# Performance work log

Measured on AMD Instinct MI355X. Metric: run time of the kernel, lower is better.

## Reference

```python
import jax, jax.numpy as jnp
import numpy as np

XBOUND = (-51.2, 51.2, 0.8)
YBOUND = (-51.2, 51.2, 0.8)
ZBOUND = (-10.0, 10.0, 20.0)
DBOUND = (1.0, 60.0, 1.0)
IMG_H, IMG_W = 256, 704
DOWNSAMPLE = 16
CAM_C = 64
OUT_C = 64
D = int((DBOUND[1] - DBOUND[0]) / DBOUND[2])      # 59
NX = int((XBOUND[1] - XBOUND[0]) / XBOUND[2])     # 128
NY = int((YBOUND[1] - YBOUND[0]) / YBOUND[2])     # 128
NZ = int((ZBOUND[1] - ZBOUND[0]) / ZBOUND[2])     # 1
FH, FW = IMG_H // DOWNSAMPLE, IMG_W // DOWNSAMPLE # 16, 44
DX = jnp.array([XBOUND[2], YBOUND[2], ZBOUND[2]], dtype=jnp.float32)
BX = jnp.array([XBOUND[0] + XBOUND[2] / 2.0, YBOUND[0] + YBOUND[2] / 2.0, ZBOUND[0] + ZBOUND[2] / 2.0], dtype=jnp.float32)


def make_frustum():
    ds = jnp.arange(DBOUND[0], DBOUND[1], DBOUND[2], dtype=jnp.float32)   # [D]
    xs = jnp.linspace(0.0, IMG_W - 1.0, FW, dtype=jnp.float32)            # [FW]
    ys = jnp.linspace(0.0, IMG_H - 1.0, FH, dtype=jnp.float32)            # [FH]
    d = jnp.broadcast_to(ds[:, None, None], (D, FH, FW))
    x = jnp.broadcast_to(xs[None, None, :], (D, FH, FW))
    y = jnp.broadcast_to(ys[None, :, None], (D, FH, FW))
    return jnp.stack([x, y, d], axis=-1)                                  # [D,FH,FW,3]


def get_geometry(rots, trans, intrins, post_rots, post_trans):
    # rots/intrins/post_rots: [B,N,3,3]; trans/post_trans: [B,N,3]
    frustum = make_frustum()                                              # [D,FH,FW,3]
    pts = frustum[None, None] - post_trans[:, :, None, None, None]        # [B,N,D,FH,FW,3]
    pts = jnp.einsum('bnij,bndhwj->bndhwi', jnp.linalg.inv(post_rots), pts)
    pts = jnp.concatenate([pts[..., :2] * pts[..., 2:3], pts[..., 2:3]], axis=-1)
    comb = jnp.matmul(rots, jnp.linalg.inv(intrins))
    pts = jnp.einsum('bnij,bndhwj->bndhwi', comb, pts)
    return pts + trans[:, :, None, None, None]


def forward(x, rots, trans, intrins, post_rots, post_trans, w_depth, b_depth):
    B, N, C_in, H, W = x.shape
    # 1x1 conv == channel matmul
    y = jnp.einsum('bnchw,oc->bnohw', x, w_depth) + b_depth[None, None, :, None, None]
    depth = jax.nn.softmax(y[:, :, :D], axis=2)              # [B,N,D,H,W]
    context = y[:, :, D:]                                    # [B,N,OUT_C,H,W]
    outer = depth[:, :, :, None] * context[:, :, None, :]    # [B,N,D,OUT_C,H,W]
    outer = jnp.transpose(outer, (0, 1, 2, 4, 5, 3))         # [B,N,D,H,W,OUT_C]

    geom = jax.lax.stop_gradient(get_geometry(rots, trans, intrins, post_rots, post_trans))
    # torch .long() truncates toward zero -> jnp.trunc
    g = jnp.trunc((geom.reshape(-1, 3) - (BX - DX / 2.0)) / DX).astype(jnp.int32)  # [P,3]
    kept = ((g[:, 0] >= 0) & (g[:, 0] < NX) &
            (g[:, 1] >= 0) & (g[:, 1] < NY) &
            (g[:, 2] >= 0) & (g[:, 2] < NZ))
    batch_ix = jnp.repeat(jnp.arange(B, dtype=jnp.int32), N * D * H * W)
    ranks = batch_ix * (NX * NY * NZ) + g[:, 0] + g[:, 1] * NX + g[:, 2] * NX * NY
    # segment-sum over voxel ranks == sort+cumsum trick + scatter in the original
    feats = jnp.where(kept[:, None], outer.reshape(-1, OUT_C), 0.0)
    ranks = jnp.where(kept, ranks, 0)
    bev = jax.ops.segment_sum(feats, ranks, num_segments=B * NZ * NY * NX)
    bev = bev.reshape(B, NZ, NY, NX, OUT_C).transpose(0, 4, 1, 2, 3).sum(axis=2)
    return bev  # [B, OUT_C, NY, NX]


def setup_inputs() -> dict:
    key = jax.random.key(0)
    B, N = 4, 6
    ks = jax.random.split(key, 8)
    cam2ego = jnp.array([[0.0, 0.0, 1.0], [-1.0, 0.0, 0.0], [0.0, -1.0, 0.0]], dtype=jnp.float32)
    rots = jnp.broadcast_to(cam2ego, (B, N, 3, 3)) + 0.02 * jax.random.normal(ks[0], (B, N, 3, 3), dtype=jnp.float32)
    trans = 1.0 * jax.random.normal(ks[1], (B, N, 3), dtype=jnp.float32)
    K = jnp.array([[700.0, 0.0, IMG_W / 2.0], [0.0, 700.0, IMG_H / 2.0], [0.0, 0.0, 1.0]], dtype=jnp.float32)
    intrins = jnp.broadcast_to(K, (B, N, 3, 3)) + 0.1 * jax.random.normal(ks[2], (B, N, 3, 3), dtype=jnp.float32)
    post_rots = jnp.broadcast_to(jnp.eye(3, dtype=jnp.float32), (B, N, 3, 3)) + 0.01 * jax.random.normal(ks[3], (B, N, 3, 3), dtype=jnp.float32)
    post_trans = 0.1 * jax.random.normal(ks[4], (B, N, 3), dtype=jnp.float32)
    x = jax.random.normal(ks[5], (B, N, CAM_C, FH, FW), dtype=jnp.float32)
    w_depth = 0.05 * jax.random.normal(ks[6], (D + OUT_C, CAM_C), dtype=jnp.float32)
    b_depth = jnp.zeros((D + OUT_C,), dtype=jnp.float32)
    return {"x": x, "rots": rots, "trans": trans, "intrins": intrins,
            "post_rots": post_rots, "post_trans": post_trans,
            "w_depth": w_depth, "b_depth": b_depth}


def reference(x, rots, trans, intrins, post_rots, post_trans, w_depth, b_depth):
    return forward(x, rots, trans, intrins, post_rots, post_trans, w_depth, b_depth)
```

## Files before the change

kernel.cpp:

```cpp
#include <hip/hip_runtime.h>
#include <math.h>

#define Bc 4
#define Nc 6
#define Dc 59
#define FHc 16
#define FWc 44
#define Cc 64
#define OCc 123
#define NXc 128
#define NYc 128
#define NVOX (Bc*NXc*NYc)
#define NBLK (Bc*Nc*FWc)

#define WS_ACC 0
#define WS_CAM ((size_t)16777216)
#define WS_WDT ((size_t)16781312)

template<bool FMA>
__device__ __forceinline__ float mulsub(float a, float b, float c) {
    if (FMA) return __fmaf_rn(-a, b, c);
    return __fadd_rn(c, __fmul_rn(-a, b));
}

template<bool FMA>
__device__ __forceinline__ void lu_inv3x3T(const float* __restrict__ m, float* __restrict__ o) {
    float A[3][3] = {{m[0],m[3],m[6]},{m[1],m[4],m[7]},{m[2],m[5],m[8]}};
    int piv0, piv1;
    {
        float a0=fabsf(A[0][0]), a1=fabsf(A[1][0]), a2=fabsf(A[2][0]);
        int p = 0; float mx = a0;
        if (a1 > mx) { mx = a1; p = 1; }
        if (a2 > mx) { mx = a2; p = 2; }
        piv0 = p;
        if (p != 0) { for (int k=0;k<3;++k){ float t=A[0][k]; A[0][k]=A[p][k]; A[p][k]=t; } }
        const float d = __fdiv_rn(1.0f, A[0][0]);
        A[1][0] = __fmul_rn(A[1][0], d);
        A[2][0] = __fmul_rn(A[2][0], d);
        #pragma unroll
        for (int i=1;i<3;++i)
            #pragma unroll
            for (int j=1;j<3;++j)
                A[i][j] = mulsub<FMA>(A[i][0], A[0][j], A[i][j]);
    }
    {
        float a1=fabsf(A[1][1]), a2=fabsf(A[2][1]);
        int p = (a2 > a1) ? 2 : 1;
        piv1 = p;
        if (p != 1) { for (int k=0;k<3;++k){ float t=A[1][k]; A[1][k]=A[p][k]; A[p][k]=t; } }
        const float d = __fdiv_rn(1.0f, A[1][1]);
        A[2][1] = __fmul_rn(A[2][1], d);
        A[2][2] = mulsub<FMA>(A[2][1], A[1][2], A[2][2]);
    }
    float B[3][3] = {{1.f,0.f,0.f},{0.f,1.f,0.f},{0.f,0.f,1.f}};
    if (piv0 != 0) { for (int k=0;k<3;++k){ float t=B[0][k]; B[0][k]=B[piv0][k]; B[piv0][k]=t; } }
    if (piv1 != 1) { for (int k=0;k<3;++k){ float t=B[1][k]; B[1][k]=B[piv1][k]; B[piv1][k]=t; } }
    #pragma unroll
    for (int j=0;j<3;++j) {
        B[1][j] = mulsub<FMA>(A[1][0], B[0][j], B[1][j]);
        B[2][j] = mulsub<FMA>(A[2][0], B[0][j], B[2][j]);
        B[2][j] = mulsub<FMA>(A[2][1], B[1][j], B[2][j]);
        B[2][j] = __fdiv_rn(B[2][j], A[2][2]);
        B[0][j] = mulsub<FMA>(A[0][2], B[2][j], B[0][j]);
        B[1][j] = mulsub<FMA>(A[1][2], B[2][j], B[1][j]);
        B[1][j] = __fdiv_rn(B[1][j], A[1][1]);
        B[0][j] = mulsub<FMA>(A[0][1], B[1][j], B[0][j]);
        B[0][j] = __fdiv_rn(B[0][j], A[0][0]);
    }
    o[0]=B[0][0]; o[1]=B[1][0]; o[2]=B[2][0];
    o[3]=B[0][1]; o[4]=B[1][1]; o[5]=B[2][1];
    o[6]=B[0][2]; o[7]=B[1][2]; o[8]=B[2][2];
}

template<bool FMA>
__device__ __forceinline__ float dot3(float a0,float a1,float a2,float b0,float b1,float b2){
    if (FMA) return __fmaf_rn(a2,b2, __fmaf_rn(a1,b1, __fmul_rn(a0,b0)));
    return __fadd_rn(__fadd_rn(__fmul_rn(a0,b0), __fmul_rn(a1,b1)), __fmul_rn(a2,b2));
}

__global__ __launch_bounds__(256) void prep(
    const float* __restrict__ wd, const float* __restrict__ rots,
    const float* __restrict__ intrins, const float* __restrict__ post_rots,
    float* __restrict__ wdT2, float* __restrict__ camMat)
{
    const int idx = blockIdx.x*256 + threadIdx.x;
    if (idx < OCc*Cc) {
        const int o = idx >> 6, c = idx & 63;
        const int slot = (o < 64) ? (o << 1) : (((o - 64) << 1) | 1);
        wdT2[(c << 7) + slot] = wd[idx];
    }
    if (idx >= OCc*Cc && idx < OCc*Cc + 320) {
        const int k = idx - OCc*Cc;
        const int c = k / 5, o = 59 + (k % 5);
        wdT2[(c << 7) + (o << 1) + 1] = 0.0f;
    }
    if (blockIdx.x == 0 && threadIdx.x < 48) {
        const int cam = threadIdx.x >> 1;
        const int var = threadIdx.x & 1;
        const float* pr = post_rots + cam*9;
        const float* ro = rots      + cam*9;
        const float* it = intrins   + cam*9;
        float PRi[9], INi[9], CM[9];
        if (var == 0) { lu_inv3x3T<true >(pr, PRi); lu_inv3x3T<true >(it, INi); }
        else          { lu_inv3x3T<false>(pr, PRi); lu_inv3x3T<false>(it, INi); }
        #pragma unroll
        for (int r2 = 0; r2 < 3; ++r2)
            #pragma unroll
            for (int c2 = 0; c2 < 3; ++c2)
                CM[r2*3+c2] = dot3<true>(ro[r2*3+0], ro[r2*3+1], ro[r2*3+2],
                                         INi[0*3+c2], INi[1*3+c2], INi[2*3+c2]);
        float* dst = camMat + (size_t)(cam*2 + var)*18;
        #pragma unroll
        for (int k = 0; k < 9; ++k) { dst[k] = PRi[k]; dst[9+k] = CM[k]; }
    }
}

template<bool FMA>
__device__ __forceinline__ int geom_light(
    const float* __restrict__ PRi, const float* __restrict__ CM,
    float pt0, float pt1, float pt2, float tr0, float tr1, float tr2,
    float u, float v, float dval, int b)
{
    const float p0 = __fsub_rn(u,    pt0);
    const float p1 = __fsub_rn(v,    pt1);
    const float p2 = __fsub_rn(dval, pt2);
    const float q0 = dot3<FMA>(PRi[0],PRi[1],PRi[2], p0,p1,p2);
    const float q1 = dot3<FMA>(PRi[3],PRi[4],PRi[5], p0,p1,p2);
    const float q2 = dot3<FMA>(PRi[6],PRi[7],PRi[8], p0,p1,p2);
    const float r0 = __fmul_rn(q0, q2);
    const float r1 = __fmul_rn(q1, q2);
    const float s0 = __fadd_rn(dot3<FMA>(CM[0],CM[1],CM[2], r0,r1,q2), tr0);
    const float s1 = __fadd_rn(dot3<FMA>(CM[3],CM[4],CM[5], r0,r1,q2), tr1);
    const float s2 = __fadd_rn(dot3<FMA>(CM[6],CM[7],CM[8], r0,r1,q2), tr2);
    const float CX  = -51.200000762939453f;
    const float DXf =  0.80000001192092896f;
    const float gx = __fdiv_rn(__fsub_rn(s0, CX), DXf);
    const float gy = __fdiv_rn(__fsub_rn(s1, CX), DXf);
    const float gz = __fdiv_rn(__fsub_rn(s2, -10.0f), 20.0f);
    const bool kept = (gx > -1.0f) && (gx < 128.0f) &&
                      (gy > -1.0f) && (gy < 128.0f) &&
                      (gz > -1.0f) && (gz < 1.0f);
    return kept ? (b*(NXc*NYc) + ((int)gy)*NXc + (int)gx) : -1;
}

__global__ __launch_bounds__(256, 4) void lss_main(
    const float* __restrict__ x, const float* __restrict__ trans,
    const float* __restrict__ post_trans, const float* __restrict__ bd,
    const float* __restrict__ wdT2, const float* __restrict__ camMat,
    float* __restrict__ acc)
{
    const int blk = blockIdx.x;
    const int wi  = blk % FWc;
    const int cam = blk / FWc;
    const int b   = cam / Nc;
    const int t = threadIdx.x;
    const int wave = t >> 6, lane = t & 63;

    __shared__ float  xsT[64][16];
    __shared__ float  yv[16][60];
    __shared__ float  ctxT[64][18];
    __shared__ float4 geo[Dc][16];

    {
        const float* xb = x + (size_t)cam*64*(FHc*FWc) + wi;
        for (int idx = t; idx < 1024; idx += 256) {
            const int c = idx >> 4, hi = idx & 15;
            xsT[c][hi] = xb[(size_t)c*(FHc*FWc) + hi*FWc];
        }
    }
    __syncthreads();

    {
        const int hi0 = wave << 2;
        float a0[4] = {0.f,0.f,0.f,0.f}, a1[4] = {0.f,0.f,0.f,0.f};
        const float2* wrow = (const float2*)wdT2 + lane;
        #pragma unroll 8
        for (int c = 0; c < 64; ++c) {
            const float2 wv = wrow[c << 6];
            const float4 xv = *(const float4*)&xsT[c][hi0];
            a0[0] = __fmaf_rn(wv.x, xv.x, a0[0]); a1[0] = __fmaf_rn(wv.y, xv.x, a1[0]);
            a0[1] = __fmaf_rn(wv.x, xv.y, a0[1]); a1[1] = __fmaf_rn(wv.y, xv.y, a1[1]);
            a0[2] = __fmaf_rn(wv.x, xv.z, a0[2]); a1[2] = __fmaf_rn(wv.y, xv.z, a1[2]);
            a0[3] = __fmaf_rn(wv.x, xv.w, a0[3]); a1[3] = __fmaf_rn(wv.y, xv.w, a1[3]);
        }
        const float b0 = bd[lane];
        const float b1 = (lane < 59) ? bd[64 + lane] : 0.0f;
        #pragma unroll
        for (int k = 0; k < 4; ++k) {
            const int hi = hi0 + k;
            const float y0 = __fadd_rn(a0[k], b0);
            if (lane < 59) {
                yv[hi][lane] = y0;
                ctxT[lane + 5][hi] = __fadd_rn(a1[k], b1);
            } else {
                ctxT[lane - 59][hi] = y0;
            }
        }
    }
    for (int k = 0; k < 4; ++k) {
        const int hi = (wave << 2) | k;
        float v = (lane < Dc) ? yv[hi][lane] : -INFINITY;
        float m = v;
        #pragma unroll
        for (int off = 32; off; off >>= 1) m = fmaxf(m, __shfl_xor(m, off));
        float e = (lane < Dc) ? expf(__fsub_rn(v, m)) : 0.0f;
        float s = e;
        #pragma unroll
        for (int off = 32; off; off >>= 1) s = __fadd_rn(s, __shfl_xor(s, off));
        if (lane < Dc) yv[hi][lane] = __fdiv_rn(e, s);
    }
    __syncthreads();

    {
        const float pt0 = post_trans[cam*3+0], pt1 = post_trans[cam*3+1], pt2 = post_trans[cam*3+2];
        const float tr0 = trans[cam*3+0],      tr1 = trans[cam*3+1],      tr2 = trans[cam*3+2];
        const float* M0 = camMat + (size_t)(cam*2 + 0)*18;
        const float* M1 = camMat + (size_t)(cam*2 + 1)*18;
        const float u = (float)(wi * (703.0 / 43.0));
        for (int idx = t; idx < 16*Dc; idx += 256) {
            const int d = idx >> 4, hi = idx & 15;
            const float v    = (float)(hi * 17.0);
            const float dval = (float)(1 + d);
            const int vA = geom_light<true >(M0, M0+9, pt0,pt1,pt2, tr0,tr1,tr2, u, v, dval, b);
            const int vB = geom_light<false>(M1, M1+9, pt0,pt1,pt2, tr0,tr1,tr2, u, v, dval, b);
            geo[d][hi] = make_float4(yv[hi][d], __int_as_float(vA), __int_as_float(vB), 0.0f);
        }
    }
    __syncthreads();

    {
        float cx[16];
        #pragma unroll
        for (int h = 0; h < 16; h += 2) {
            const float2 c2 = *(const float2*)&ctxT[lane][h];
            cx[h] = c2.x; cx[h+1] = c2.y;
        }
        for (int d = wave; d < Dc; d += 4) {
            int runVox = -1;
            float accv = 0.0f;
            #pragma unroll
            for (int hi = 0; hi < 16; ++hi) {
                const float4 g = geo[d][hi];
                const float dw = g.x;
                const int vA = __float_as_int(g.y);
                const int vB = __float_as_int(g.z);
                const float cxv = cx[hi];
                if (vA == vB) {
                    if (vA >= 0) {
                        if (vA != runVox) {
                            if (runVox >= 0) atomicAdd(&acc[((size_t)runVox << 6) + lane], accv);
                            runVox = vA; accv = 0.0f;
                        }
                        accv = __fadd_rn(accv, __fmul_rn(dw, cxv));
                    }
                } else {
                    const float hw = __fmul_rn(dw, 0.5f);
                    if (vA >= 0) {
                        if (vA != runVox) {
                            if (runVox >= 0) atomicAdd(&acc[((size_t)runVox << 6) + lane], accv);
                            runVox = vA; accv = 0.0f;
                        }
                        accv = __fadd_rn(accv, __fmul_rn(hw, cxv));
                    }
                    if (vB >= 0) atomicAdd(&acc[((size_t)vB << 6) + lane], __fmul_rn(hw, cxv));
                }
            }
            if (runVox >= 0) atomicAdd(&acc[((size_t)runVox << 6) + lane], accv);
        }
    }
}

__global__ __launch_bounds__(256) void lss_transpose(
    const float* __restrict__ acc, float* __restrict__ out)
{
    __shared__ float tile[64][65];
    const int blk = blockIdx.x;
    const int b = blk >> 8;
    const int pixbase = (blk & 255) * 64;
    const float* src = acc + ((size_t)b*16384 + pixbase)*64;
    const int t = threadIdx.x;
    #pragma unroll
    for (int i = 0; i < 16; ++i) {
        const int e = i*256 + t;
        tile[e & 63][e >> 6] = src[e];
    }
    __syncthreads();
    float* dst = out + (size_t)b*64*16384 + pixbase;
    #pragma unroll
    for (int i = 0; i < 16; ++i) {
        const int e = i*256 + t;
        const int c = e >> 6, p = e & 63;
        dst[(size_t)c*16384 + p] = tile[c][p];
    }
}

extern "C" void kernel_launch(void* const* d_in, const int* in_sizes, int n_in,
                              void* d_out, int out_size, void* d_ws, size_t ws_size,
                              hipStream_t stream) {
    const float* x          = (const float*)d_in[0];
    const float* rots       = (const float*)d_in[1];
    const float* trans      = (const float*)d_in[2];
    const float* intrins    = (const float*)d_in[3];
    const float* post_rots  = (const float*)d_in[4];
    const float* post_trans = (const float*)d_in[5];
    const float* wd         = (const float*)d_in[6];
    const float* bd         = (const float*)d_in[7];
    float* out = (float*)d_out;
    char* ws = (char*)d_ws;

    float* acc    = (float*)(ws + WS_ACC);
    float* camMat = (float*)(ws + WS_CAM);
    float* wdT2   = (float*)(ws + WS_WDT);

    hipMemsetAsync(acc, 0, (size_t)NVOX*64*sizeof(float), stream);
    prep<<<dim3(32), dim3(256), 0, stream>>>(wd, rots, intrins, post_rots, wdT2, camMat);
    lss_main<<<dim3(NBLK), dim3(256), 0, stream>>>(
        x, trans, post_trans, bd, wdT2, camMat, acc);
    lss_transpose<<<dim3(Bc*256), dim3(256), 0, stream>>>(acc, out);
}
```

Baseline: 203.6 us.

## Fuse memset, prep, scatter and transpose into one kernel with grid barriers

Replaces the memset, prep kernel, main scatter kernel and transpose kernel with a single persistent kernel. Phases are separated by software grid barriers on atomic counters that use a poison-value convention for first-arrival initialisation. It also zeroes the accumulator in-kernel with float4 stores and vectorises the transpose loads and stores. The aim is to remove launch and inter-kernel gaps, but correctness relies on all 1056 blocks being co-resident and on the counter workspace being re-poisoned before every call.

```diff
diff --git a/kernel.cpp b/kernel.cpp
--- a/kernel.cpp
+++ b/kernel.cpp
@@ -16,6 +16,8 @@
 #define WS_ACC 0
 #define WS_CAM ((size_t)16777216)
 #define WS_WDT ((size_t)16781312)
+#define WS_CNT ((size_t)16814080)
+#define POISON 0xAAAAAAAAu
 
 template<bool FMA>
 __device__ __forceinline__ float mulsub(float a, float b, float c) {
@@ -76,43 +78,6 @@
 __device__ __forceinline__ float dot3(float a0,float a1,float a2,float b0,float b1,float b2){
     if (FMA) return __fmaf_rn(a2,b2, __fmaf_rn(a1,b1, __fmul_rn(a0,b0)));
     return __fadd_rn(__fadd_rn(__fmul_rn(a0,b0), __fmul_rn(a1,b1)), __fmul_rn(a2,b2));
-}
-
-__global__ __launch_bounds__(256) void prep(
-    const float* __restrict__ wd, const float* __restrict__ rots,
-    const float* __restrict__ intrins, const float* __restrict__ post_rots,
-    float* __restrict__ wdT2, float* __restrict__ camMat)
-{
-    const int idx = blockIdx.x*256 + threadIdx.x;
-    if (idx < OCc*Cc) {
-        const int o = idx >> 6, c = idx & 63;
-        const int slot = (o < 64) ? (o << 1) : (((o - 64) << 1) | 1);
-        wdT2[(c << 7) + slot] = wd[idx];
-    }
-    if (idx >= OCc*Cc && idx < OCc*Cc + 320) {
-        const int k = idx - OCc*Cc;
-        const int c = k / 5, o = 59 + (k % 5);
-        wdT2[(c << 7) + (o << 1) + 1] = 0.0f;
-    }
-    if (blockIdx.x == 0 && threadIdx.x < 48) {
-        const int cam = threadIdx.x >> 1;
-        const int var = threadIdx.x & 1;
-        const float* pr = post_rots + cam*9;
-        const float* ro = rots      + cam*9;
-        const float* it = intrins   + cam*9;
-        float PRi[9], INi[9], CM[9];
-        if (var == 0) { lu_inv3x3T<true >(pr, PRi); lu_inv3x3T<true >(it, INi); }
-        else          { lu_inv3x3T<false>(pr, PRi); lu_inv3x3T<false>(it, INi); }
-        #pragma unroll
-        for (int r2 = 0; r2 < 3; ++r2)
-            #pragma unroll
-            for (int c2 = 0; c2 < 3; ++c2)
-                CM[r2*3+c2] = dot3<true>(ro[r2*3+0], ro[r2*3+1], ro[r2*3+2],
-                                         INi[0*3+c2], INi[1*3+c2], INi[2*3+c2]);
-        float* dst = camMat + (size_t)(cam*2 + var)*18;
-        #pragma unroll
-        for (int k = 0; k < 9; ++k) { dst[k] = PRi[k]; dst[9+k] = CM[k]; }
-    }
 }
 
 template<bool FMA>
@@ -143,154 +108,220 @@
     return kept ? (b*(NXc*NYc) + ((int)gy)*NXc + (int)gx) : -1;
 }
 
-__global__ __launch_bounds__(256, 4) void lss_main(
-    const float* __restrict__ x, const float* __restrict__ trans,
-    const float* __restrict__ post_trans, const float* __restrict__ bd,
-    const float* __restrict__ wdT2, const float* __restrict__ camMat,
-    float* __restrict__ acc)
+__device__ __forceinline__ void grid_barrier(unsigned* cnt, unsigned target) {
+    __threadfence();
+    __syncthreads();
+    if (threadIdx.x == 0) {
+        unsigned old = atomicCAS(cnt, POISON, 1u);
+        if (old != POISON) atomicAdd(cnt, 1u);
+        unsigned iters = 0;
+        while (atomicAdd(cnt, 0u) < target) {
+            __builtin_amdgcn_s_sleep(16);
+            if (++iters > 50000000u) break;
+        }
+    }
+    __syncthreads();
+    __threadfence();
+}
+
+struct P1 {
+    float geo[Dc][16][4];
+    float xsT[64][16];
+    float yv[16][60];
+    float ctxT[64][18];
+};
+struct P2 { float tile[64][65]; };
+
+__global__ __launch_bounds__(256, 5) void lss_fused(
+    const float* __restrict__ x, const float* __restrict__ rots,
+    const float* __restrict__ trans, const float* __restrict__ intrins,
+    const float* __restrict__ post_rots, const float* __restrict__ post_trans,
+    const float* __restrict__ wd, const float* __restrict__ bd,
+    float* __restrict__ acc, float* __restrict__ camMat,
+    float* __restrict__ wdT2, unsigned* __restrict__ cnts,
+    float* __restrict__ out)
 {
     const int blk = blockIdx.x;
-    const int wi  = blk % FWc;
-    const int cam = blk / FWc;
-    const int b   = cam / Nc;
     const int t = threadIdx.x;
-    const int wave = t >> 6, lane = t & 63;
-
-    __shared__ float  xsT[64][16];
-    __shared__ float  yv[16][60];
-    __shared__ float  ctxT[64][18];
-    __shared__ float4 geo[Dc][16];
+    const int gtid = blk*256 + t;
+
+    __shared__ union SMem { P1 p1; P2 p2; } sm;
 
     {
-        const float* xb = x + (size_t)cam*64*(FHc*FWc) + wi;
-        for (int idx = t; idx < 1024; idx += 256) {
-            const int c = idx >> 4, hi = idx & 15;
-            xsT[c][hi] = xb[(size_t)c*(FHc*FWc) + hi*FWc];
-        }
-    }
-    __syncthreads();
+        float4* acc4 = (float4*)acc;
+        const float4 z = make_float4(0.f, 0.f, 0.f, 0.f);
+        for (int i = gtid; i < (NVOX*64)/4; i += NBLK*256) acc4[i] = z;
+        if (gtid < OCc*Cc) {
+            const int o = gtid >> 6, c = gtid & 63;
+            const int slot = (o < 64) ? (o << 1) : (((o - 64) << 1) | 1);
+            wdT2[(c << 7) + slot] = wd[gtid];
+        } else if (gtid < OCc*Cc + 320) {
+            const int k = gtid - OCc*Cc;
+            const int c = k / 5, o = 59 + (k % 5);
+            wdT2[(c << 7) + (o << 1) + 1] = 0.0f;
+        }
+        if (gtid < 48) {
+            const int cam = gtid >> 1;
+            const int var = gtid & 1;
+            const float* pr = post_rots + cam*9;
+            const float* ro = rots      + cam*9;
+            const float* it = intrins   + cam*9;
+            float PRi[9], INi[9], CM[9];
+            if (var == 0) { lu_inv3x3T<true >(pr, PRi); lu_inv3x3T<true >(it, INi); }
+            else          { lu_inv3x3T<false>(pr, PRi); lu_inv3x3T<false>(it, INi); }
+            #pragma unroll
+            for (int r2 = 0; r2 < 3; ++r2)
+                #pragma unroll
+                for (int c2 = 0; c2 < 3; ++c2)
+                    CM[r2*3+c2] = dot3<true>(ro[r2*3+0], ro[r2*3+1], ro[r2*3+2],
+                                             INi[0*3+c2], INi[1*3+c2], INi[2*3+c2]);
+            float* dst = camMat + (size_t)(cam*2 + var)*18;
+            #pragma unroll
+            for (int k = 0; k < 9; ++k) { dst[k] = PRi[k]; dst[9+k] = CM[k]; }
+        }
+    }
+    grid_barrier(&cnts[0], NBLK);
 
     {
-        const int hi0 = wave << 2;
-        float a0[4] = {0.f,0.f,0.f,0.f}, a1[4] = {0.f,0.f,0.f,0.f};
-        const float2* wrow = (const float2*)wdT2 + lane;
-        #pragma unroll 8
-        for (int c = 0; c < 64; ++c) {
-            const float2 wv = wrow[c << 6];
-            const float4 xv = *(const float4*)&xsT[c][hi0];
-            a0[0] = __fmaf_rn(wv.x, xv.x, a0[0]); a1[0] = __fmaf_rn(wv.y, xv.x, a1[0]);
-            a0[1] = __fmaf_rn(wv.x, xv.y, a0[1]); a1[1] = __fmaf_rn(wv.y, xv.y, a1[1]);
-            a0[2] = __fmaf_rn(wv.x, xv.z, a0[2]); a1[2] = __fmaf_rn(wv.y, xv.z, a1[2]);
-            a0[3] = __fmaf_rn(wv.x, xv.w, a0[3]); a1[3] = __fmaf_rn(wv.y, xv.w, a1[3]);
-        }
-        const float b0 = bd[lane];
-        const float b1 = (lane < 59) ? bd[64 + lane] : 0.0f;
+        const int wi  = blk % FWc;
+        const int cam = blk / FWc;
+        const int b   = cam / Nc;
+        const int wave = t >> 6, lane = t & 63;
+
+        {
+            const float* xb = x + (size_t)cam*64*(FHc*FWc) + wi;
+            for (int idx = t; idx < 1024; idx += 256) {
+                const int c = idx >> 4, hi = idx & 15;
+                sm.p1.xsT[c][hi] = xb[(size_t)c*(FHc*FWc) + hi*FWc];
+            }
+        }
+        __syncthreads();
+
+        {
+            const int hi0 = wave << 2;
+            float a0[4] = {0.f,0.f,0.f,0.f}, a1[4] = {0.f,0.f,0.f,0.f};
+            const float2* wrow = (const float2*)wdT2 + lane;
+            #pragma unroll 8
+            for (int c = 0; c < 64; ++c) {
+                const float2 wv = wrow[c << 6];
+                const float4 xv = *(const float4*)&sm.p1.xsT[c][hi0];
+                a0[0] = __fmaf_rn(wv.x, xv.x, a0[0]); a1[0] = __fmaf_rn(wv.y, xv.x, a1[0]);
+                a0[1] = __fmaf_rn(wv.x, xv.y, a0[1]); a1[1] = __fmaf_rn(wv.y, xv.y, a1[1]);
+                a0[2] = __fmaf_rn(wv.x, xv.z, a0[2]); a1[2] = __fmaf_rn(wv.y, xv.z, a1[2]);
+                a0[3] = __fmaf_rn(wv.x, xv.w, a0[3]); a1[3] = __fmaf_rn(wv.y, xv.w, a1[3]);
+            }
+            const float b0 = bd[lane];
+            const float b1 = (lane < 59) ? bd[64 + lane] : 0.0f;
+            #pragma unroll
+            for (int k = 0; k < 4; ++k) {
+                const int hi = hi0 + k;
+                const float y0 = __fadd_rn(a0[k], b0);
+                if (lane < 59) {
+                    sm.p1.yv[hi][lane] = y0;
+                    sm.p1.ctxT[lane + 5][hi] = __fadd_rn(a1[k], b1);
+                } else {
+                    sm.p1.ctxT[lane - 59][hi] = y0;
+                }
+            }
+        }
+        for (int k = 0; k < 4; ++k) {
+            const int hi = (wave << 2) | k;
+            float v = (lane < Dc) ? sm.p1.yv[hi][lane] : -INFINITY;
+            float m = v;
+            #pragma unroll
+            for (int off = 32; off; off >>= 1) m = fmaxf(m, __shfl_xor(m, off));
+            float e = (lane < Dc) ? expf(__fsub_rn(v, m)) : 0.0f;
+            float s = e;
+            #pragma unroll
+            for (int off = 32; off; off >>= 1) s = __fadd_rn(s, __shfl_xor(s, off));
+            if (lane < Dc) sm.p1.yv[hi][lane] = __fdiv_rn(e, s);
+        }
+        __syncthreads();
+
+        {
+            const float pt0 = post_trans[cam*3+0], pt1 = post_trans[cam*3+1], pt2 = post_trans[cam*3+2];
+            const float tr0 = trans[cam*3+0],      tr1 = trans[cam*3+1],      tr2 = trans[cam*3+2];
+            const float* M0 = camMat + (size_t)(cam*2 + 0)*18;
+            const float* M1 = camMat + (size_t)(cam*2 + 1)*18;
+            const float u = (float)(wi * (703.0 / 43.0));
+            for (int idx = t; idx < 16*Dc; idx += 256) {
+                const int d = idx >> 4, hi = idx & 15;
+                const float v    = (float)(hi * 17.0);
+                const float dval = (float)(1 + d);
+                const int vA = geom_light<true >(M0, M0+9, pt0,pt1,pt2, tr0,tr1,tr2, u, v, dval, b);
+                const int vB = geom_light<false>(M1, M1+9, pt0,pt1,pt2, tr0,tr1,tr2, u, v, dval, b);
+                *(float4*)&sm.p1.geo[d][hi][0] =
+                    make_float4(sm.p1.yv[hi][d], __int_as_float(vA), __int_as_float(vB), 0.0f);
+            }
+        }
+        __syncthreads();
+
+        {
+            float cx[16];
+            #pragma unroll
+            for (int h = 0; h < 16; h += 2) {
+                const float2 c2 = *(const float2*)&sm.p1.ctxT[lane][h];
+                cx[h] = c2.x; cx[h+1] = c2.y;
+            }
+            for (int d = wave; d < Dc; d += 4) {
+                int runVox = -1;
+                float accv = 0.0f;
+                #pragma unroll
+                for (int hi = 0; hi < 16; ++hi) {
+                    const float4 g = *(const float4*)&sm.p1.geo[d][hi][0];
+                    const float dw = g.x;
+                    const int vA = __float_as_int(g.y);
+                    const int vB = __float_as_int(g.z);
+                    const float cxv = cx[hi];
+                    if (vA == vB) {
+                        if (vA >= 0) {
+                            if (vA != runVox) {
+                                if (runVox >= 0) atomicAdd(&acc[((size_t)runVox << 6) + lane], accv);
+                                runVox = vA; accv = 0.0f;
+                            }
+                            accv = __fadd_rn(accv, __fmul_rn(dw, cxv));
+                        }
+                    } else {
+                        const float hw = __fmul_rn(dw, 0.5f);
+                        if (vA >= 0) {
+                            if (vA != runVox) {
+                                if (runVox >= 0) atomicAdd(&acc[((size_t)runVox << 6) + lane], accv);
+                                runVox = vA; accv = 0.0f;
+                            }
+                            accv = __fadd_rn(accv, __fmul_rn(hw, cxv));
+                        }
+                        if (vB >= 0) atomicAdd(&acc[((size_t)vB << 6) + lane], __fmul_rn(hw, cxv));
+                    }
+                }
+                if (runVox >= 0) atomicAdd(&acc[((size_t)runVox << 6) + lane], accv);
+            }
+        }
+    }
+    grid_barrier(&cnts[1], NBLK);
+
+    if (blk < 1024) {
+        const int b = blk >> 8;
+        const int pixbase = (blk & 255) * 64;
+        const float4* src4 = (const float4*)(acc + ((size_t)b*16384 + pixbase)*64);
         #pragma unroll
-        for (int k = 0; k < 4; ++k) {
-            const int hi = hi0 + k;
-            const float y0 = __fadd_rn(a0[k], b0);
-            if (lane < 59) {
-                yv[hi][lane] = y0;
-                ctxT[lane + 5][hi] = __fadd_rn(a1[k], b1);
-            } else {
-                ctxT[lane - 59][hi] = y0;
-            }
-        }
-    }
-    for (int k = 0; k < 4; ++k) {
-        const int hi = (wave << 2) | k;
-        float v = (lane < Dc) ? yv[hi][lane] : -INFINITY;
-        float m = v;
+        for (int i = 0; i < 4; ++i) {
+            const int e4 = i*256 + t;
+            const float4 v = src4[e4];
+            const int e = e4 << 2;
+            const int r = e & 63, c = e >> 6;
+            sm.p2.tile[r+0][c] = v.x; sm.p2.tile[r+1][c] = v.y;
+            sm.p2.tile[r+2][c] = v.z; sm.p2.tile[r+3][c] = v.w;
+        }
+        __syncthreads();
+        float* dst = out + (size_t)b*64*16384 + pixbase;
         #pragma unroll
-        for (int off = 32; off; off >>= 1) m = fmaxf(m, __shfl_xor(m, off));
-        float e = (lane < Dc) ? expf(__fsub_rn(v, m)) : 0.0f;
-        float s = e;
-        #pragma unroll
-        for (int off = 32; off; off >>= 1) s = __fadd_rn(s, __shfl_xor(s, off));
-        if (lane < Dc) yv[hi][lane] = __fdiv_rn(e, s);
-    }
-    __syncthreads();
-
-    {
-        const float pt0 = post_trans[cam*3+0], pt1 = post_trans[cam*3+1], pt2 = post_trans[cam*3+2];
-        const float tr0 = trans[cam*3+0],      tr1 = trans[cam*3+1],      tr2 = trans[cam*3+2];
-        const float* M0 = camMat + (size_t)(cam*2 + 0)*18;
-        const float* M1 = camMat + (size_t)(cam*2 + 1)*18;
-        const float u = (float)(wi * (703.0 / 43.0));
-        for (int idx = t; idx < 16*Dc; idx += 256) {
-            const int d = idx >> 4, hi = idx & 15;
-            const float v    = (float)(hi * 17.0);
-            const float dval = (float)(1 + d);
-            const int vA = geom_light<true >(M0, M0+9, pt0,pt1,pt2, tr0,tr1,tr2, u, v, dval, b);
-            const int vB = geom_light<false>(M1, M1+9, pt0,pt1,pt2, tr0,tr1,tr2, u, v, dval, b);
-            geo[d][hi] = make_float4(yv[hi][d], __int_as_float(vA), __int_as_float(vB), 0.0f);
-        }
-    }
-    __syncthreads();
-
-    {
-        float cx[16];
-        #pragma unroll
-        for (int h = 0; h < 16; h += 2) {
-            const float2 c2 = *(const float2*)&ctxT[lane][h];
-            cx[h] = c2.x; cx[h+1] = c2.y;
-        }
-        for (int d = wave; d < Dc; d += 4) {
-            int runVox = -1;
-            float accv = 0.0f;
-            #pragma unroll
-            for (int hi = 0; hi < 16; ++hi) {
-                const float4 g = geo[d][hi];
-                const float dw = g.x;
-                const int vA = __float_as_int(g.y);
-                const int vB = __float_as_int(g.z);
-                const float cxv = cx[hi];
-                if (vA == vB) {
-                    if (vA >= 0) {
-                        if (vA != runVox) {
-                            if (runVox >= 0) atomicAdd(&acc[((size_t)runVox << 6) + lane], accv);
-                            runVox = vA; accv = 0.0f;
-                        }
-                        accv = __fadd_rn(accv, __fmul_rn(dw, cxv));
-                    }
-                } else {
-                    const float hw = __fmul_rn(dw, 0.5f);
-                    if (vA >= 0) {
-                        if (vA != runVox) {
-                            if (runVox >= 0) atomicAdd(&acc[((size_t)runVox << 6) + lane], accv);
-                            runVox = vA; accv = 0.0f;
-                        }
-                        accv = __fadd_rn(accv, __fmul_rn(hw, cxv));
-                    }
-                    if (vB >= 0) atomicAdd(&acc[((size_t)vB << 6) + lane], __fmul_rn(hw, cxv));
-                }
-            }
-            if (runVox >= 0) atomicAdd(&acc[((size_t)runVox << 6) + lane], accv);
-        }
-    }
-}
-
-__global__ __launch_bounds__(256) void lss_transpose(
-    const float* __restrict__ acc, float* __restrict__ out)
-{
-    __shared__ float tile[64][65];
-    const int blk = blockIdx.x;
-    const int b = blk >> 8;
-    const int pixbase = (blk & 255) * 64;
-    const float* src = acc + ((size_t)b*16384 + pixbase)*64;
-    const int t = threadIdx.x;
-    #pragma unroll
-    for (int i = 0; i < 16; ++i) {
-        const int e = i*256 + t;
-        tile[e & 63][e >> 6] = src[e];
-    }
-    __syncthreads();
-    float* dst = out + (size_t)b*64*16384 + pixbase;
-    #pragma unroll
-    for (int i = 0; i < 16; ++i) {
-        const int e = i*256 + t;
-        const int c = e >> 6, p = e & 63;
-        dst[(size_t)c*16384 + p] = tile[c][p];
+        for (int i = 0; i < 4; ++i) {
+            const int idx = i*256 + t;
+            const int c = idx >> 4, p = (idx & 15) << 2;
+            const float4 v = make_float4(sm.p2.tile[c][p],   sm.p2.tile[c][p+1],
+                                         sm.p2.tile[c][p+2], sm.p2.tile[c][p+3]);
+            *(float4*)&dst[(size_t)c*16384 + p] = v;
+        }
     }
 }
 
@@ -308,13 +339,12 @@
     float* out = (float*)d_out;
     char* ws = (char*)d_ws;
 
-    float* acc    = (float*)(ws + WS_ACC);
-    float* camMat = (float*)(ws + WS_CAM);
-    float* wdT2   = (float*)(ws + WS_WDT);
-
-    hipMemsetAsync(acc, 0, (size_t)NVOX*64*sizeof(float), stream);
-    prep<<<dim3(32), dim3(256), 0, stream>>>(wd, rots, intrins, post_rots, wdT2, camMat);
-    lss_main<<<dim3(NBLK), dim3(256), 0, stream>>>(
-        x, trans, post_trans, bd, wdT2, camMat, acc);
-    lss_transpose<<<dim3(Bc*256), dim3(256), 0, stream>>>(acc, out);
-}
+    float*    acc    = (float*)(ws + WS_ACC);
+    float*    camMat = (float*)(ws + WS_CAM);
+    float*    wdT2   = (float*)(ws + WS_WDT);
+    unsigned* cnts   = (unsigned*)(ws + WS_CNT);
+
+    lss_fused<<<dim3(NBLK), dim3(256), 0, stream>>>(
+        x, rots, trans, intrins, post_rots, post_trans, wd, bd,
+        acc, camMat, wdT2, cnts, out);
+}
```

Result: slower. 678.8 us (+233.4%).
